# Kernel tuning notes

Measured on AMD Instinct MI355X. Metric: run time of the kernel, lower is better.

The kernel has to match this reference:

```python
import jax, jax.numpy as jnp
import numpy as np

V, E, H, M = 50000, 256, 512, 100   # vocab, emb_dim, hid_dim, mlp_hid_dim
H2 = H // 2                          # per-direction GRU size
B, S, T = 64, 400, 25                # batch, src_len, max_trg_len
EOS = 2                              # vocab['</s>'] -> CE weight 0


def _gru(x, h, Wih, Whh, bih, bhh):
    # torch GRU/GRUCell gate math
    gi = x @ Wih.T + bih
    gh = h @ Whh.T + bhh
    ir, iz, inn = jnp.split(gi, 3, axis=-1)
    hr, hz, hn = jnp.split(gh, 3, axis=-1)
    r = jax.nn.sigmoid(ir + hr)
    z = jax.nn.sigmoid(iz + hz)
    n = jnp.tanh(inn + r * hn)
    return (1.0 - z) * n + z * h


def _run_gru(xs, Wih, Whh, bih, bhh, reverse):
    # xs: [S, B, E] -> ys [S, B, H2], hT [B, H2]
    if reverse:
        xs = xs[::-1]
    h0 = jnp.zeros((xs.shape[1], Whh.shape[1]), xs.dtype)
    def step(h, x):
        h2 = _gru(x, h, Wih, Whh, bih, bhh)
        return h2, h2
    hT, ys = jax.lax.scan(step, h0, xs)
    if reverse:
        ys = ys[::-1]
    return ys, hT


def _model(src, trg, params):
    (emb, Wih_f, Whh_f, bih_f, bhh_f, Wih_b, Whh_b, bih_b, bhh_b,
     W1, b1, W2, b2, Wd, bd, We, be, Wo, bo,
     Wih_c, Whh_c, bih_c, bhh_c, Wv, bv) = params
    # ---- encode ----
    embeds = emb[src].transpose(1, 0, 2)                    # [S, B, E]
    ys_f, hf = _run_gru(embeds, Wih_f, Whh_f, bih_f, bhh_f, False)
    ys_b, hb = _run_gru(embeds, Wih_b, Whh_b, bih_b, bhh_b, True)
    states = jnp.concatenate([ys_f, ys_b], axis=-1)         # [S, B, H]
    enc_hidden = jnp.concatenate([hf, hb], axis=-1)         # [B, H]
    sgate = jax.nn.sigmoid(states @ W1.T + b1 + (enc_hidden @ W2.T + b2)[None])
    states = states * sgate
    enc_proj = states @ We.T + be                           # [S, B, M] (loop-invariant)
    # ---- decode (training path, weighted CE per step) ----
    def dec_step(carry, tok):
        h, loss = carry
        wemb = emb[tok]                                     # [B, E]
        e = jnp.tanh((h @ Wd.T + bd)[None] + enc_proj) @ Wo.T + bo  # [S, B, 1]
        a = jax.nn.softmax(e, axis=0)
        c = jnp.sum(a * states, axis=0)                     # [B, H]
        h2 = _gru(jnp.concatenate([c, wemb], axis=-1), h, Wih_c, Whh_c, bih_c, bhh_c)
        logits = h2 @ Wv.T + bv                             # [B, V]
        logp = jax.nn.log_softmax(logits, axis=-1)
        nll = -jnp.take_along_axis(logp, tok[:, None], axis=1)[:, 0]
        w = (tok != EOS).astype(logits.dtype)               # CE class weight mask
        step_loss = jnp.sum(w * nll) / jnp.sum(w)           # torch weighted-mean CE
        return (h2, loss + step_loss), None
    toks = trg[:, : T - 1].T                                # [T-1, B]
    (_, loss), _ = jax.lax.scan(dec_step, (enc_hidden, jnp.zeros((), states.dtype)), toks)
    return loss / B


def setup_inputs() -> dict:
    key = jax.random.key(0)
    ks = jax.random.split(key, 16)
    def p(k, shape, s=0.05):
        return jax.random.normal(k, shape, jnp.float32) * s
    z = lambda n: jnp.zeros((n,), jnp.float32)
    return {
        "src": jax.random.randint(ks[0], (B, S), 0, V, dtype=jnp.int32),
        "trg": jax.random.randint(ks[1], (B, T), 0, V, dtype=jnp.int32),
        "emb": p(ks[2], (V, E)),
        "Wih_f": p(ks[3], (3 * H2, E)), "Whh_f": p(ks[4], (3 * H2, H2)),
        "bih_f": z(3 * H2), "bhh_f": z(3 * H2),
        "Wih_b": p(ks[5], (3 * H2, E)), "Whh_b": p(ks[6], (3 * H2, H2)),
        "bih_b": z(3 * H2), "bhh_b": z(3 * H2),
        "W1": p(ks[7], (H, H)), "b1": z(H),
        "W2": p(ks[8], (H, H)), "b2": z(H),
        "Wd": p(ks[9], (M, H)), "bd": z(M),
        "We": p(ks[10], (M, H)), "be": z(M),
        "Wo": p(ks[11], (1, M)), "bo": z(1),
        "Wih_c": p(ks[12], (3 * H, H + E)), "Whh_c": p(ks[13], (3 * H, H)),
        "bih_c": z(3 * H), "bhh_c": z(3 * H),
        "Wv": p(ks[14], (V, H)), "bv": z(V),
    }


def reference(src, trg, emb, Wih_f, Whh_f, bih_f, bhh_f, Wih_b, Whh_b, bih_b, bhh_b,
              W1, b1, W2, b2, Wd, bd, We, be, Wo, bo,
              Wih_c, Whh_c, bih_c, bhh_c, Wv, bv):
    params = (emb, Wih_f, Whh_f, bih_f, bhh_f, Wih_b, Whh_b, bih_b, bhh_b,
              W1, b1, W2, b2, Wd, bd, We, be, Wo, bo,
              Wih_c, Whh_c, bih_c, bhh_c, Wv, bv)
    return _model(src, trg, params)
```

## Files before the change

### kernel.cpp

```cpp
#include <hip/hip_runtime.h>

typedef __bf16 bf16;
typedef bf16 bf16x2 __attribute__((ext_vector_type(2)));
typedef bf16 bf16x4 __attribute__((ext_vector_type(4)));
typedef bf16 bf16x8 __attribute__((ext_vector_type(8)));
typedef float f32x4 __attribute__((ext_vector_type(4)));

#define DEVFN __device__ __forceinline__

constexpr int cV = 50000, cE = 256, cH = 512, cM = 100, cH2 = 256;
constexpr int cB = 64, cS = 400, cT = 25, cEOS = 2;
constexpr int cSB = cS * cB;
constexpr int cG2 = 3 * cH2;
constexpr int cGP = 772;
constexpr int cKcat = 1280;
constexpr int cN4 = 2048;
constexpr int cNTV = (cV + 63) / 64;
constexpr int cTD = cT - 1;
constexpr int cVT = cV / 16;

constexpr size_t OFF_WV = 0;
constexpr size_t N_WV = (size_t)cV * cH;
constexpr size_t OFF_WIHF = OFF_WV + N_WV;
constexpr size_t N_WIH = (size_t)cG2 * cE;
constexpr size_t OFF_WHHF = OFF_WIHF + N_WIH;
constexpr size_t N_WHH = (size_t)cG2 * cH2;
constexpr size_t OFF_WIHB = OFF_WHHF + N_WHH;
constexpr size_t OFF_WHHB = OFF_WIHB + N_WIH;
constexpr size_t OFF_W1 = OFF_WHHB + N_WHH;
constexpr size_t N_WSQ = (size_t)cH * cH;
constexpr size_t OFF_W2 = OFF_W1 + N_WSQ;
constexpr size_t OFF_WE = OFF_W2 + N_WSQ;
constexpr size_t N_WE = (size_t)cM * cH;
constexpr size_t TOT_W = OFF_WE + N_WE;

constexpr int NB_CVT = (int)(TOT_W / 4 / 256);
constexpr int NB_WP = cN4 * cKcat / 256;
constexpr int NB_GATHER = cSB * cE / 256;
constexpr int NB_PREP = NB_CVT + NB_WP + NB_GATHER;

struct GArgs {
  const bf16* A; const bf16* Bw; const float* bias;
  float* outF; bf16* outBf;
  const float* auxF; const bf16* auxBf;
  int M, N, K, ldo;
};

DEVFN float sigm(float x) { return 1.f / (1.f + __expf(-x)); }
DEVFN float tanh_f(float x) {
  float e2 = __expf(2.f * x);
  return 1.f - 2.f / (e2 + 1.f);
}

DEVFN void gload_lds16(const void* g, void* l) {
  __builtin_amdgcn_global_load_lds(
      (const __attribute__((address_space(1))) void*)g,
      (__attribute__((address_space(3))) void*)l, 16, 0, 0);
}

template <int EPI>
__global__ __launch_bounds__(256) void gemm64_k(GArgs g) {
  const int tid = threadIdx.x;
  const int w = blockIdx.x * 4 + (tid >> 6);
  const int tM = g.M >> 6;
  const int tN = (g.N + 63) >> 6;
  if (w >= tM * tN) return;
  const int im = w % tM, in = w / tM;
  const int m0 = im << 6, n0 = in << 6;
  const int lane = tid & 63, lr = lane & 15, lh = lane >> 4;

  f32x4 acc[4][4];
#pragma unroll
  for (int i = 0; i < 4; ++i)
#pragma unroll
    for (int j = 0; j < 4; ++j)
#pragma unroll
      for (int r = 0; r < 4; ++r) acc[i][j][r] = 0.f;

  bf16x8 bz;
#pragma unroll
  for (int q = 0; q < 8; ++q) bz[q] = (bf16)0.f;

  const int K = g.K;
#pragma unroll 2
  for (int k0 = 0; k0 < K; k0 += 32) {
    bf16x8 av[4], bw[4];
#pragma unroll
    for (int mt = 0; mt < 4; ++mt)
      av[mt] = *(const bf16x8*)(g.A + (size_t)(m0 + mt * 16 + lr) * K + k0 + lh * 8);
#pragma unroll
    for (int nt = 0; nt < 4; ++nt) {
      int row = n0 + nt * 16 + lr;
      bw[nt] = (row < g.N) ? *(const bf16x8*)(g.Bw + (size_t)row * K + k0 + lh * 8) : bz;
    }
#pragma unroll
    for (int mt = 0; mt < 4; ++mt)
#pragma unroll
      for (int nt = 0; nt < 4; ++nt)
        acc[mt][nt] = __builtin_amdgcn_mfma_f32_16x16x32_bf16(av[mt], bw[nt], acc[mt][nt], 0, 0, 0);
  }

#pragma unroll
  for (int mt = 0; mt < 4; ++mt) {
#pragma unroll
    for (int nt = 0; nt < 4; ++nt) {
      const int n = n0 + nt * 16 + lr;
      if (n < g.N) {
        const float bia = g.bias[n];
#pragma unroll
        for (int r = 0; r < 4; ++r) {
          const int m = m0 + mt * 16 + lh * 4 + r;
          float v = acc[mt][nt][r] + bia;
          if constexpr (EPI == 0) {
            g.outF[(size_t)m * g.ldo + n] = v;
          } else {
            float sg = sigm(v + g.auxF[(size_t)(m & 63) * g.ldo + n]);
            float st = (float)g.auxBf[(size_t)m * g.ldo + n];
            g.outBf[(size_t)m * g.ldo + n] = (bf16)(sg * st);
          }
        }
      }
    }
  }
}

__global__ void prep_k(const float* __restrict__ wv, const float* __restrict__ wihf,
                       const float* __restrict__ whhf, const float* __restrict__ wihb,
                       const float* __restrict__ whhb, const float* __restrict__ w1,
                       const float* __restrict__ w2, const float* __restrict__ we,
                       bf16* __restrict__ dst,
                       const float* __restrict__ Wih_c, const float* __restrict__ Whh_c,
                       const float* __restrict__ bih_c, const float* __restrict__ bhh_c,
                       bf16* __restrict__ Wp, float* __restrict__ bp,
                       const int* __restrict__ src, const float* __restrict__ emb,
                       bf16* __restrict__ embeds) {
  const int blk = blockIdx.x, tid = threadIdx.x;

  if (blk < NB_CVT) {
    size_t i = ((size_t)blk * 256 + tid) * 4;
    if (i >= TOT_W) return;
    if (i < OFF_WIHF) {
      float4 v = *(const float4*)(wv + i);
      size_t row = i >> 9, col = i & 511;
      size_t tile = row >> 4, lr = row & 15, kc = col >> 5, lh = (col >> 3) & 3, e = col & 7;
      size_t d = ((tile * 16 + kc) * 64 + lr * 4 + lh) * 8 + e;
      bf16x4 o;
      o[0] = (bf16)v.x; o[1] = (bf16)v.y; o[2] = (bf16)v.z; o[3] = (bf16)v.w;
      *(bf16x4*)(dst + d) = o;
      return;
    }
    const float* s;
    size_t off;
    if (i < OFF_WHHF) { s = wihf; off = OFF_WIHF; }
    else if (i < OFF_WIHB) { s = whhf; off = OFF_WHHF; }
    else if (i < OFF_WHHB) { s = wihb; off = OFF_WIHB; }
    else if (i < OFF_W1) { s = whhb; off = OFF_WHHB; }
    else if (i < OFF_W2) { s = w1; off = OFF_W1; }
    else if (i < OFF_WE) { s = w2; off = OFF_W2; }
    else { s = we; off = OFF_WE; }
    float4 v = *(const float4*)(s + (i - off));
    bf16x4 o;
    o[0] = (bf16)v.x; o[1] = (bf16)v.y; o[2] = (bf16)v.z; o[3] = (bf16)v.w;
    *(bf16x4*)(dst + i) = o;
    return;
  }
  if (blk < NB_CVT + NB_WP) {
    int i = (blk - NB_CVT) * 256 + tid;
    int j = i / cKcat, c = i % cKcat;
    int bi = j >> 6, gg = (j >> 4) & 3, idx = j & 15;
    int u = bi * 16 + idx;
    float v;
    if (gg == 0) v = (c < 768) ? Wih_c[(size_t)u * 768 + c] : Whh_c[(size_t)u * 512 + (c - 768)];
    else if (gg == 1) v = (c < 768) ? Wih_c[(size_t)(512 + u) * 768 + c] : Whh_c[(size_t)(512 + u) * 512 + (c - 768)];
    else if (gg == 2) v = (c < 768) ? Wih_c[(size_t)(1024 + u) * 768 + c] : 0.f;
    else v = (c < 768) ? 0.f : Whh_c[(size_t)(1024 + u) * 512 + (c - 768)];
    {
      size_t tile = (size_t)j >> 4, lr = j & 15, kc = c >> 5, lh = (c >> 3) & 3, e = c & 7;
      Wp[((tile * 40 + kc) * 64 + lr * 4 + lh) * 8 + e] = (bf16)v;
    }
    if (c == 0) {
      float bb;
      if (gg == 0) bb = bih_c[u] + bhh_c[u];
      else if (gg == 1) bb = bih_c[512 + u] + bhh_c[512 + u];
      else if (gg == 2) bb = bih_c[1024 + u];
      else bb = bhh_c[1024 + u];
      bp[j] = bb;
    }
    return;
  }
  {
    int i = (blk - NB_CVT - NB_WP) * 256 + tid;
    int e = i & 255;
    int sb = i >> 8;
    int s = sb >> 6, b = sb & 63;
    int tok = src[b * cS + s];
    embeds[i] = (bf16)emb[(size_t)tok * cE + e];
  }
}

__global__ __launch_bounds__(256) void gi2_k(const bf16* __restrict__ embeds,
                                             const bf16* __restrict__ WihF,
                                             const float* __restrict__ bihF,
                                             float* __restrict__ giF,
                                             const bf16* __restrict__ WihB,
                                             const float* __restrict__ bihB,
                                             float* __restrict__ giB) {
  int blk = blockIdx.x;
  const bf16* Bw;
  const float* bias;
  float* outF;
  if (blk < 1200) { Bw = WihF; bias = bihF; outF = giF; }
  else { blk -= 1200; Bw = WihB; bias = bihB; outF = giB; }
  const int tid = threadIdx.x;
  const int w = blk * 4 + (tid >> 6);
  const int im = w % 400, in = w / 400;
  const int m0 = im << 6, n0 = in << 6;
  const int lane = tid & 63, lr = lane & 15, lh = lane >> 4;

  f32x4 acc[4][4];
#pragma unroll
  for (int i = 0; i < 4; ++i)
#pragma unroll
    for (int j = 0; j < 4; ++j)
#pragma unroll
      for (int r = 0; r < 4; ++r) acc[i][j][r] = 0.f;

#pragma unroll 2
  for (int k0 = 0; k0 < cE; k0 += 32) {
    bf16x8 av[4], bw[4];
#pragma unroll
    for (int mt = 0; mt < 4; ++mt)
      av[mt] = *(const bf16x8*)(embeds + (size_t)(m0 + mt * 16 + lr) * cE + k0 + lh * 8);
#pragma unroll
    for (int nt = 0; nt < 4; ++nt)
      bw[nt] = *(const bf16x8*)(Bw + (size_t)(n0 + nt * 16 + lr) * cE + k0 + lh * 8);
#pragma unroll
    for (int mt = 0; mt < 4; ++mt)
#pragma unroll
      for (int nt = 0; nt < 4; ++nt)
        acc[mt][nt] = __builtin_amdgcn_mfma_f32_16x16x32_bf16(av[mt], bw[nt], acc[mt][nt], 0, 0, 0);
  }
#pragma unroll
  for (int mt = 0; mt < 4; ++mt)
#pragma unroll
    for (int nt = 0; nt < 4; ++nt) {
      const int n = n0 + nt * 16 + lr;
      const float bia = bias[n];
#pragma unroll
      for (int r = 0; r < 4; ++r) {
        const int m = m0 + mt * 16 + lh * 4 + r;
        outF[(size_t)m * cG2 + n] = acc[mt][nt][r] + bia;
      }
    }
}

__global__ __launch_bounds__(512, 1) void enc_rnn_k(
    const bf16* __restrict__ WhhF, const bf16* __restrict__ WhhB,
    const float* __restrict__ giF, const float* __restrict__ giB,
    const float* __restrict__ bhhF, const float* __restrict__ bhhB,
    bf16* __restrict__ hdec0_bf, float* __restrict__ hdec0_f,
    bf16* __restrict__ states) {
  const int blk = blockIdx.x;
  const int dir = blk >> 2;
  const int bc = blk & 3;
  const bf16* Whh = dir ? WhhB : WhhF;
  const float* gi = dir ? giB : giF;
  const float* bhh = dir ? bhhB : bhhF;

  const int tid = threadIdx.x;
  const int lane = tid & 63, w = tid >> 6;
  const int lr = lane & 15, lh = lane >> 4;
  const int u0 = w * 32;

  bf16x8 Bf[6][8];
  float bh[6];
#pragma unroll
  for (int gg = 0; gg < 3; ++gg)
#pragma unroll
    for (int ut = 0; ut < 2; ++ut) {
      int nbase = gg * 256 + u0 + ut * 16;
#pragma unroll
      for (int kf = 0; kf < 8; ++kf)
        Bf[gg * 2 + ut][kf] = *(const bf16x8*)(Whh + (size_t)(nbase + lr) * 256 + kf * 32 + lh * 8);
      bh[gg * 2 + ut] = bhh[nbase + lr];
    }

  __shared__ float gilds[2][16][cGP];
  __shared__ bf16 hs[2][16][264];

  auto prefetch = [&](int t2) {
    if (t2 >= cS) return;
    const int s2 = dir ? (cS - 1 - t2) : t2;
    const int buf = t2 & 1;
#pragma unroll
    for (int rr2 = 0; rr2 < 2; ++rr2) {
      const int row = w * 2 + rr2;
      const char* srcb = (const char*)(gi + ((size_t)s2 * cB + bc * 16 + row) * cG2);
      char* dstb = (char*)&gilds[buf][row][0];
#pragma unroll
      for (int c = 0; c < 3; ++c)
        gload_lds16(srcb + c * 1024 + lane * 16, dstb + c * 1024);
    }
  };

  float hreg[2][4];
#pragma unroll
  for (int ut = 0; ut < 2; ++ut)
#pragma unroll
    for (int r = 0; r < 4; ++r) hreg[ut][r] = 0.f;

  prefetch(0);
  for (int i = tid; i < 16 * 264; i += 512) ((bf16*)hs[0])[i] = (bf16)0.f;
  __syncthreads();

  for (int t = 0; t < cS; ++t) {
    const int buf = t & 1, nbuf = buf ^ 1;
    prefetch(t + 1);

    bf16x8 av[8];
#pragma unroll
    for (int kf = 0; kf < 8; ++kf)
      av[kf] = *(const bf16x8*)(&hs[buf][lr][kf * 32 + lh * 8]);

    float gir[2][4], giz[2][4], gin[2][4];
#pragma unroll
    for (int ut = 0; ut < 2; ++ut) {
      const int u = u0 + ut * 16 + lr;
#pragma unroll
      for (int r = 0; r < 4; ++r) {
        const int b = lh * 4 + r;
        gir[ut][r] = gilds[buf][b][u];
        giz[ut][r] = gilds[buf][b][256 + u];
        gin[ut][r] = gilds[buf][b][512 + u];
      }
    }

    f32x4 acc[6];
#pragma unroll
    for (int j = 0; j < 6; ++j)
#pragma unroll
      for (int r = 0; r < 4; ++r) acc[j][r] = 0.f;

#pragma unroll
    for (int kf = 0; kf < 8; ++kf)
#pragma unroll
      for (int nt = 0; nt < 6; ++nt)
        acc[nt] = __builtin_amdgcn_mfma_f32_16x16x32_bf16(av[kf], Bf[nt][kf], acc[nt], 0, 0, 0);

#pragma unroll
    for (int ut = 0; ut < 2; ++ut) {
      const int u = u0 + ut * 16 + lr;
#pragma unroll
      for (int r = 0; r < 4; ++r) {
        const int b = lh * 4 + r;
        float rr = sigm(gir[ut][r] + acc[ut][r] + bh[ut]);
        float zz = sigm(giz[ut][r] + acc[2 + ut][r] + bh[2 + ut]);
        float nn = tanh_f(gin[ut][r] + rr * (acc[4 + ut][r] + bh[4 + ut]));
        float hnew = (1.f - zz) * nn + zz * hreg[ut][r];
        hreg[ut][r] = hnew;
        hs[nbuf][b][u] = (bf16)hnew;
      }
    }

    __syncthreads();

    {
      const int s_src = dir ? (cS - 1 - t) : t;
      const int row = tid >> 5, c8 = tid & 31;
      bf16x8 v = *(const bf16x8*)(&hs[nbuf][row][c8 * 8]);
      *(bf16x8*)(states + ((size_t)s_src * cB + bc * 16 + row) * cH + dir * 256 + c8 * 8) = v;
    }
  }

#pragma unroll
  for (int ut = 0; ut < 2; ++ut)
#pragma unroll
    for (int r = 0; r < 4; ++r) {
      const int b = bc * 16 + lh * 4 + r;
      const int col = dir * 256 + u0 + ut * 16 + lr;
      hdec0_f[(size_t)b * cH + col] = hreg[ut][r];
      hdec0_bf[(size_t)b * cH + col] = (bf16)hreg[ut][r];
    }
}

__global__ __launch_bounds__(256) void projtransp_k(const bf16* __restrict__ statesg,
                                                    const bf16* __restrict__ We_b,
                                                    const float* __restrict__ be,
                                                    float* __restrict__ epT,
                                                    bf16* __restrict__ sgT) {
  __shared__ bf16 tile[64][520];
  const int tid = threadIdx.x;
  if (blockIdx.x < 200) {
    const int w = blockIdx.x * 4 + (tid >> 6);
    const int im = w % 400, in = w / 400;
    const int m0 = im << 6, n0 = in << 6;
    const int lane = tid & 63, lr = lane & 15, lh = lane >> 4;
    f32x4 acc[4][4];
#pragma unroll
    for (int i = 0; i < 4; ++i)
#pragma unroll
      for (int j = 0; j < 4; ++j)
#pragma unroll
        for (int r = 0; r < 4; ++r) acc[i][j][r] = 0.f;
    bf16x8 bz;
#pragma unroll
    for (int q = 0; q < 8; ++q) bz[q] = (bf16)0.f;
#pragma unroll 2
    for (int k0 = 0; k0 < cH; k0 += 32) {
      bf16x8 av[4], bw[4];
#pragma unroll
      for (int mt = 0; mt < 4; ++mt)
        av[mt] = *(const bf16x8*)(statesg + (size_t)(m0 + mt * 16 + lr) * cH + k0 + lh * 8);
#pragma unroll
      for (int nt = 0; nt < 4; ++nt) {
        int row = n0 + nt * 16 + lr;
        bw[nt] = (row < cM) ? *(const bf16x8*)(We_b + (size_t)row * cH + k0 + lh * 8) : bz;
      }
#pragma unroll
      for (int mt = 0; mt < 4; ++mt)
#pragma unroll
        for (int nt = 0; nt < 4; ++nt)
          acc[mt][nt] = __builtin_amdgcn_mfma_f32_16x16x32_bf16(av[mt], bw[nt], acc[mt][nt], 0, 0, 0);
    }
#pragma unroll
    for (int mt = 0; mt < 4; ++mt)
#pragma unroll
      for (int nt = 0; nt < 4; ++nt) {
        const int n = n0 + nt * 16 + lr;
        if (n < cM) {
          const float bia = be[n];
#pragma unroll
          for (int r = 0; r < 4; ++r) {
            const int m = m0 + mt * 16 + lh * 4 + r;
            const int bb = m & 63, s = m >> 6;
            epT[((size_t)bb * cM + n) * cS + s] = acc[mt][nt][r] + bia;
          }
        }
      }
    return;
  }
  const int b = blockIdx.x - 200;
  for (int s0 = 0; s0 < cS; s0 += 64) {
    __syncthreads();
    for (int c = tid; c < 64 * 64; c += 256) {
      int row = c >> 6, col = c & 63;
      *(bf16x8*)(&tile[row][col * 8]) =
          *(const bf16x8*)(statesg + ((size_t)(s0 + row) * cB + b) * cH + col * 8);
    }
    __syncthreads();
    for (int c = tid; c < 512 * 8; c += 256) {
      int k = c >> 3, sc = c & 7;
      bf16x8 v;
#pragma unroll
      for (int j = 0; j < 8; ++j) v[j] = tile[sc * 8 + j][k];
      *(bf16x8*)(sgT + ((size_t)b * cH + k) * cS + s0 + sc * 8) = v;
    }
  }
}

__global__ __launch_bounds__(512) void attn_k(
    const bf16* __restrict__ hin, const float* __restrict__ Wd, const float* __restrict__ bd,
    const float* __restrict__ Wo, const float* __restrict__ bo,
    const float* __restrict__ epT, const bf16* __restrict__ sgT,
    const float* __restrict__ emb, const int* __restrict__ trg, int t,
    bf16* __restrict__ xh) {
  const int b = blockIdx.x, tid = threadIdx.x;
  const int lane = tid & 63, wid = tid >> 6;
  __shared__ float hsh[512];
  __shared__ float dsh[100];
  __shared__ float esh[400];
  __shared__ float red[32];
  __shared__ float wos[100];

  if (tid < 100) wos[tid] = Wo[tid];
  hsh[tid] = (float)hin[b * 512 + tid];
  __syncthreads();

  for (int j = wid; j < 100; j += 8) {
    const float* wr = Wd + (size_t)j * 512 + lane * 8;
    float a = 0.f;
#pragma unroll
    for (int q = 0; q < 8; ++q) a += wr[q] * hsh[lane * 8 + q];
#pragma unroll
    for (int m = 1; m < 64; m <<= 1) a += __shfl_xor(a, m);
    if (lane == 0) dsh[j] = a + bd[j];
  }
  __syncthreads();

  float e0 = -3.4e38f;
  if (tid < 400) {
    const float* p = epT + (size_t)b * cM * cS + tid;
    float a0 = 0.f, a1 = 0.f, a2 = 0.f, a3 = 0.f;
#pragma unroll
    for (int j = 0; j < 100; j += 4) {
      a0 += wos[j + 0] * tanh_f(dsh[j + 0] + p[(j + 0) * cS]);
      a1 += wos[j + 1] * tanh_f(dsh[j + 1] + p[(j + 1) * cS]);
      a2 += wos[j + 2] * tanh_f(dsh[j + 2] + p[(j + 2) * cS]);
      a3 += wos[j + 3] * tanh_f(dsh[j + 3] + p[(j + 3) * cS]);
    }
    e0 = bo[0] + ((a0 + a1) + (a2 + a3));
  }
  float mx = e0;
#pragma unroll
  for (int m = 1; m < 64; m <<= 1) mx = fmaxf(mx, __shfl_xor(mx, m));
  if (lane == 0) red[wid] = mx;
  __syncthreads();
  mx = red[0];
#pragma unroll
  for (int q = 1; q < 8; ++q) mx = fmaxf(mx, red[q]);

  float av = (tid < 400) ? __expf(e0 - mx) : 0.f;
  if (tid < 400) esh[tid] = av;
  float sm = av;
#pragma unroll
  for (int m = 1; m < 64; m <<= 1) sm += __shfl_xor(sm, m);
  if (lane == 0) red[8 + wid] = sm;
  __syncthreads();
  sm = red[8];
#pragma unroll
  for (int q = 1; q < 8; ++q) sm += red[8 + q];
  const float inv = 1.f / sm;

  {
    const bf16* sp = sgT + ((size_t)b * cH + tid) * cS;
    float c0 = 0.f, c1 = 0.f, c2 = 0.f, c3 = 0.f;
    for (int s = 0; s < 384; s += 32) {
      bf16x8 v0 = *(const bf16x8*)(sp + s);
      bf16x8 v1 = *(const bf16x8*)(sp + s + 8);
      bf16x8 v2 = *(const bf16x8*)(sp + s + 16);
      bf16x8 v3 = *(const bf16x8*)(sp + s + 24);
#pragma unroll
      for (int j = 0; j < 8; ++j) {
        c0 += esh[s + j] * (float)v0[j];
        c1 += esh[s + 8 + j] * (float)v1[j];
        c2 += esh[s + 16 + j] * (float)v2[j];
        c3 += esh[s + 24 + j] * (float)v3[j];
      }
    }
    {
      bf16x8 v0 = *(const bf16x8*)(sp + 384);
      bf16x8 v1 = *(const bf16x8*)(sp + 392);
#pragma unroll
      for (int j = 0; j < 8; ++j) {
        c0 += esh[384 + j] * (float)v0[j];
        c1 += esh[392 + j] * (float)v1[j];
      }
    }
    xh[(size_t)b * cKcat + tid] = (bf16)(((c0 + c1) + (c2 + c3)) * inv);
  }
  if (tid < 256) {
    const int tok = trg[b * cT + t];
    xh[(size_t)b * cKcat + 512 + tid] = (bf16)emb[(size_t)tok * cE + tid];
  }
  xh[(size_t)b * cKcat + 768 + tid] = hin[b * 512 + tid];
}

__global__ __launch_bounds__(256) void gru_k(
    const bf16* __restrict__ xh, const bf16* __restrict__ Wp, const float* __restrict__ bp,
    const float* __restrict__ hin_f, float* __restrict__ hout_f, bf16* __restrict__ hallt) {
  const int tid = threadIdx.x;
  const int lane = tid & 63, wid = tid >> 6;
  const int w = blockIdx.x * 4 + wid;
  const int n0 = w << 6, lr = lane & 15, lh = lane >> 4;
  f32x4 acc[4][4];
#pragma unroll
  for (int i = 0; i < 4; ++i)
#pragma unroll
    for (int j = 0; j < 4; ++j)
#pragma unroll
      for (int r = 0; r < 4; ++r) acc[i][j][r] = 0.f;
#pragma unroll 2
  for (int k0 = 0; k0 < cKcat; k0 += 32) {
    bf16x8 av[4], bw[4];
#pragma unroll
    for (int mt = 0; mt < 4; ++mt)
      av[mt] = *(const bf16x8*)(xh + (size_t)(mt * 16 + lr) * cKcat + k0 + lh * 8);
#pragma unroll
    for (int nt = 0; nt < 4; ++nt)
      bw[nt] = *(const bf16x8*)(Wp + (((size_t)(w * 4 + nt) * 40 + (k0 >> 5)) * 64 + lr * 4 + lh) * 8);
#pragma unroll
    for (int mt = 0; mt < 4; ++mt)
#pragma unroll
      for (int nt = 0; nt < 4; ++nt)
        acc[mt][nt] = __builtin_amdgcn_mfma_f32_16x16x32_bf16(av[mt], bw[nt], acc[mt][nt], 0, 0, 0);
  }
  const int u = (n0 >> 2) + lr;
  const float br = bp[n0 + lr];
  const float bz2 = bp[n0 + 16 + lr];
  const float bi2 = bp[n0 + 32 + lr];
  const float bh2 = bp[n0 + 48 + lr];
#pragma unroll
  for (int mt = 0; mt < 4; ++mt)
#pragma unroll
    for (int r = 0; r < 4; ++r) {
      const int bb = mt * 16 + lh * 4 + r;
      float rr = sigm(acc[mt][0][r] + br);
      float zz = sigm(acc[mt][1][r] + bz2);
      float nn = tanh_f(acc[mt][2][r] + bi2 + rr * (acc[mt][3][r] + bh2));
      float h2v = (1.f - zz) * nn + zz * hin_f[(size_t)bb * cH + u];
      hout_f[(size_t)bb * cH + u] = h2v;
      hallt[(size_t)bb * cH + u] = (bf16)h2v;
    }
}

__global__ __launch_bounds__(256) void biglogits_k(
    const bf16* __restrict__ hall, const bf16* __restrict__ WvS,
    const float* __restrict__ bv, float* __restrict__ partials) {
  const int tid = threadIdx.x;
  const int lane = tid & 63, wid = tid >> 6;
  const int im = blockIdx.x % cTD;
  const int in = (blockIdx.x / cTD) * 4 + wid;
  if (in >= cNTV) return;
  const int m0 = im << 6, lr = lane & 15, lh = lane >> 4;

  f32x4 acc[4][4];
#pragma unroll
  for (int i = 0; i < 4; ++i)
#pragma unroll
    for (int j = 0; j < 4; ++j)
#pragma unroll
      for (int r = 0; r < 4; ++r) acc[i][j][r] = 0.f;
  bf16x8 bz;
#pragma unroll
  for (int q = 0; q < 8; ++q) bz[q] = (bf16)0.f;

#pragma unroll 2
  for (int k0 = 0; k0 < cH; k0 += 32) {
    bf16x8 av[4], bw[4];
#pragma unroll
    for (int mt = 0; mt < 4; ++mt)
      av[mt] = *(const bf16x8*)(hall + (size_t)(m0 + mt * 16 + lr) * cH + k0 + lh * 8);
#pragma unroll
    for (int nt = 0; nt < 4; ++nt) {
      const int tile = in * 4 + nt;
      bw[nt] = (tile < cVT)
                   ? *(const bf16x8*)(WvS + (((size_t)tile * 16 + (k0 >> 5)) * 64 + lr * 4 + lh) * 8)
                   : bz;
    }
#pragma unroll
    for (int mt = 0; mt < 4; ++mt)
#pragma unroll
      for (int nt = 0; nt < 4; ++nt)
        acc[mt][nt] = __builtin_amdgcn_mfma_f32_16x16x32_bf16(av[mt], bw[nt], acc[mt][nt], 0, 0, 0);
  }

#pragma unroll
  for (int mt = 0; mt < 4; ++mt) {
#pragma unroll
    for (int r = 0; r < 4; ++r) {
      const int m = m0 + mt * 16 + lh * 4 + r;
      float vv[4];
      float mx = -3.4e38f;
#pragma unroll
      for (int nt = 0; nt < 4; ++nt) {
        int n = (in << 6) + nt * 16 + lr;
        float v = (n < cV) ? (acc[mt][nt][r] + bv[n]) : -3.4e38f;
        vv[nt] = v;
        mx = fmaxf(mx, v);
      }
#pragma unroll
      for (int msk = 1; msk < 16; msk <<= 1) mx = fmaxf(mx, __shfl_xor(mx, msk));
      float sm = 0.f;
#pragma unroll
      for (int nt = 0; nt < 4; ++nt) {
        int n = (in << 6) + nt * 16 + lr;
        if (n < cV) sm += __expf(vv[nt] - mx);
      }
#pragma unroll
      for (int msk = 1; msk < 16; msk <<= 1) sm += __shfl_xor(sm, msk);
      if (lr == 0) {
        float* p = partials + ((size_t)m * cNTV + in) * 2;
        p[0] = mx;
        p[1] = sm;
      }
    }
  }
}

__global__ __launch_bounds__(64) void rowloss_all_k(
    const float* __restrict__ partials, const bf16* __restrict__ hall,
    const float* __restrict__ Wv, const float* __restrict__ bv,
    const int* __restrict__ trg, float* __restrict__ rnll, float* __restrict__ rw) {
  const int m = blockIdx.x, tid = threadIdx.x;
  const int t = m >> 6, bb = m & 63;
  float mx = -3.4e38f, sm = 0.f;
  const float* pr = partials + (size_t)m * cNTV * 2;
  for (int p = tid; p < cNTV; p += 64) {
    float m2 = pr[p * 2], s2 = pr[p * 2 + 1];
    if (m2 > mx) { sm = sm * __expf(mx - m2) + s2; mx = m2; }
    else sm += s2 * __expf(m2 - mx);
  }
#pragma unroll
  for (int msk = 1; msk < 64; msk <<= 1) {
    float om = __shfl_xor(mx, msk), os = __shfl_xor(sm, msk);
    if (om > mx) { sm = sm * __expf(mx - om) + os; mx = om; }
    else sm += os * __expf(om - mx);
  }
  const int tok = trg[bb * cT + t];
  float dot = 0.f;
  {
    const float* wr = Wv + (size_t)tok * cH + tid * 8;
    const bf16* hr = hall + (size_t)m * cH + tid * 8;
    bf16x8 h8 = *(const bf16x8*)hr;
#pragma unroll
    for (int j = 0; j < 8; ++j) dot += (float)h8[j] * wr[j];
  }
#pragma unroll
  for (int msk = 1; msk < 64; msk <<= 1) dot += __shfl_xor(dot, msk);
  if (tid == 0) {
    float lse = mx + __logf(sm);
    float nll = lse - (dot + bv[tok]);
    float wgt = (tok != cEOS) ? 1.f : 0.f;
    rnll[m] = wgt * nll;
    rw[m] = wgt;
  }
}

__global__ __launch_bounds__(64) void final_loss_k(const float* __restrict__ rnll,
                                                   const float* __restrict__ rw,
                                                   float* __restrict__ out) {
  __shared__ float sl[32];
  const int t = threadIdx.x;
  if (t < cTD) {
    float a = 0.f, d = 0.f;
    for (int b = 0; b < cB; ++b) { a += rnll[t * cB + b]; d += rw[t * cB + b]; }
    sl[t] = a / d;
  }
  __syncthreads();
  if (t == 0) {
    float s = 0.f;
    for (int i = 0; i < cTD; ++i) s += sl[i];
    out[0] = s / (float)cB;
  }
}

extern "C" void kernel_launch(void* const* d_in, const int* in_sizes, int n_in,
                              void* d_out, int out_size, void* d_ws, size_t ws_size,
                              hipStream_t stream) {
  (void)in_sizes; (void)n_in; (void)out_size; (void)ws_size;
  const int* src = (const int*)d_in[0];
  const int* trg = (const int*)d_in[1];
  const float* emb = (const float*)d_in[2];
  const float* Wih_f = (const float*)d_in[3];
  const float* Whh_f = (const float*)d_in[4];
  const float* bih_f = (const float*)d_in[5];
  const float* bhh_f = (const float*)d_in[6];
  const float* Wih_b = (const float*)d_in[7];
  const float* Whh_b = (const float*)d_in[8];
  const float* bih_b = (const float*)d_in[9];
  const float* bhh_b = (const float*)d_in[10];
  const float* W1 = (const float*)d_in[11];
  const float* b1 = (const float*)d_in[12];
  const float* W2 = (const float*)d_in[13];
  const float* b2 = (const float*)d_in[14];
  const float* Wd = (const float*)d_in[15];
  const float* bd = (const float*)d_in[16];
  const float* We = (const float*)d_in[17];
  const float* be = (const float*)d_in[18];
  const float* Wo = (const float*)d_in[19];
  const float* bo = (const float*)d_in[20];
  const float* Wih_c = (const float*)d_in[21];
  const float* Whh_c = (const float*)d_in[22];
  const float* bih_c = (const float*)d_in[23];
  const float* bhh_c = (const float*)d_in[24];
  const float* Wv = (const float*)d_in[25];
  const float* bv = (const float*)d_in[26];
  float* out = (float*)d_out;

  char* ws = (char*)d_ws;
  size_t off = 0;
  auto carve = [&](size_t bytes) -> void* {
    void* p = ws + off;
    off += (bytes + 255) & ~(size_t)255;
    return p;
  };
  bf16* wcat = (bf16*)carve(TOT_W * 2);
  bf16* WvS = wcat + OFF_WV;
  bf16* Wihf_b = wcat + OFF_WIHF;
  bf16* Whhf_b = wcat + OFF_WHHF;
  bf16* Wihb_b = wcat + OFF_WIHB;
  bf16* Whhb_b = wcat + OFF_WHHB;
  bf16* W1_b = wcat + OFF_W1;
  bf16* W2_b = wcat + OFF_W2;
  bf16* We_b = wcat + OFF_WE;
  bf16* Wp_b = (bf16*)carve((size_t)cN4 * cKcat * 2);
  float* bp = (float*)carve((size_t)cN4 * 4);
  bf16* embeds = (bf16*)carve((size_t)cSB * cE * 2);
  float* gi_f = (float*)carve((size_t)cSB * cG2 * 4);
  float* gi_b = (float*)carve((size_t)cSB * cG2 * 4);
  bf16* states = (bf16*)carve((size_t)cSB * cH * 2);
  bf16* statesg = (bf16*)carve((size_t)cSB * cH * 2);
  bf16* statesgT = (bf16*)carve((size_t)cSB * cH * 2);
  bf16* hdec0_bf = (bf16*)carve((size_t)cB * cH * 2);
  float* hdec0_f = (float*)carve((size_t)cB * cH * 4);
  float* hfA = (float*)carve((size_t)cB * cH * 4);
  float* hfB = (float*)carve((size_t)cB * cH * 4);
  float* hw2 = (float*)carve((size_t)cB * cH * 4);
  float* epT = (float*)carve((size_t)cB * cM * cS * 4);
  bf16* xh = (bf16*)carve((size_t)cB * cKcat * 2);
  bf16* hall = (bf16*)carve((size_t)cTD * cB * cH * 2);
  float* partials = (float*)carve((size_t)cTD * cB * cNTV * 2 * 4);
  float* rnll = (float*)carve((size_t)cTD * cB * 4);
  float* rw = (float*)carve((size_t)cTD * cB * 4);

  prep_k<<<dim3(NB_PREP), dim3(256), 0, stream>>>(
      Wv, Wih_f, Whh_f, Wih_b, Whh_b, W1, W2, We, wcat,
      Wih_c, Whh_c, bih_c, bhh_c, Wp_b, bp, src, emb, embeds);
  gi2_k<<<dim3(2400), dim3(256), 0, stream>>>(embeds, Wihf_b, bih_f, gi_f,
                                              Wihb_b, bih_b, gi_b);
  enc_rnn_k<<<dim3(8), dim3(512), 0, stream>>>(Whhf_b, Whhb_b, gi_f, gi_b, bhh_f, bhh_b,
                                               hdec0_bf, hdec0_f, states);
  {
    GArgs ga{hdec0_bf, W2_b, b2, hw2, nullptr, nullptr, nullptr, cB, cH, cH, cH};
    gemm64_k<0><<<dim3(2), dim3(256), 0, stream>>>(ga);
  }
  {
    GArgs ga{states, W1_b, b1, nullptr, statesg, hw2, states, cSB, cH, cH, cH};
    int waves = (cSB / 64) * (cH / 64);
    gemm64_k<1><<<dim3((waves + 3) / 4), dim3(256), 0, stream>>>(ga);
  }
  projtransp_k<<<dim3(264), dim3(256), 0, stream>>>(statesg, We_b, be, epT, statesgT);

  for (int t = 0; t < cTD; ++t) {
    const bf16* hin_bf = (t == 0) ? hdec0_bf : (hall + (size_t)(t - 1) * cB * cH);
    const float* hin_f = (t == 0) ? hdec0_f : ((t & 1) ? hfA : hfB);
    float* hout_f = (t & 1) ? hfB : hfA;

    attn_k<<<dim3(cB), dim3(512), 0, stream>>>(hin_bf, Wd, bd, Wo, bo, epT, statesgT,
                                               emb, trg, t, xh);
    gru_k<<<dim3(8), dim3(256), 0, stream>>>(xh, Wp_b, bp, hin_f, hout_f,
                                             hall + (size_t)t * cB * cH);
  }

  biglogits_k<<<dim3(cTD * ((cNTV + 3) / 4)), dim3(256), 0, stream>>>(hall, WvS, bv, partials);
  rowloss_all_k<<<dim3(cTD * cB), dim3(64), 0, stream>>>(partials, hall, Wv, bv, trg, rnll, rw);
  final_loss_k<<<dim3(1), dim3(64), 0, stream>>>(rnll, rw, out);
}
```

Measured before the change: 3.677 ms.

## Overlap weight conversion with encoder RNN and store attention projection in bf16

```diff
diff --git a/kernel.cpp b/kernel.cpp
--- a/kernel.cpp
+++ b/kernel.cpp
@@ -34,10 +34,16 @@
 constexpr size_t N_WE = (size_t)cM * cH;
 constexpr size_t TOT_W = OFF_WE + N_WE;
 
-constexpr int NB_CVT = (int)(TOT_W / 4 / 256);
-constexpr int NB_WP = cN4 * cKcat / 256;
+constexpr int NB_CVT1 = (int)(4 * N_WIH / 4 / 256);
 constexpr int NB_GATHER = cSB * cE / 256;
-constexpr int NB_PREP = NB_CVT + NB_WP + NB_GATHER;
+constexpr int NB_PREP1 = NB_CVT1 + NB_GATHER;
+
+constexpr int NB_WVS = (int)(N_WV / 4 / 512);
+constexpr size_t N_TAIL = N_WSQ + N_WSQ + N_WE;
+constexpr int NB_TAIL = (int)(N_TAIL / 4 / 512);
+constexpr int NB_WP2 = cN4 * cKcat / 4 / 512;
+constexpr int NB_PREP2 = NB_WVS + NB_TAIL + NB_WP2;
+constexpr int ENC_GRID = 8 + NB_PREP2;
 
 struct GArgs {
   const bf16* A; const bf16* Bw; const float* bias;
@@ -124,72 +130,28 @@
   }
 }
 
-__global__ void prep_k(const float* __restrict__ wv, const float* __restrict__ wihf,
-                       const float* __restrict__ whhf, const float* __restrict__ wihb,
-                       const float* __restrict__ whhb, const float* __restrict__ w1,
-                       const float* __restrict__ w2, const float* __restrict__ we,
-                       bf16* __restrict__ dst,
-                       const float* __restrict__ Wih_c, const float* __restrict__ Whh_c,
-                       const float* __restrict__ bih_c, const float* __restrict__ bhh_c,
-                       bf16* __restrict__ Wp, float* __restrict__ bp,
-                       const int* __restrict__ src, const float* __restrict__ emb,
-                       bf16* __restrict__ embeds) {
+__global__ void prep1_k(const float* __restrict__ wihf, const float* __restrict__ whhf,
+                        const float* __restrict__ wihb, const float* __restrict__ whhb,
+                        bf16* __restrict__ dst,
+                        const int* __restrict__ src, const float* __restrict__ emb,
+                        bf16* __restrict__ embeds) {
   const int blk = blockIdx.x, tid = threadIdx.x;
-
-  if (blk < NB_CVT) {
-    size_t i = ((size_t)blk * 256 + tid) * 4;
-    if (i >= TOT_W) return;
-    if (i < OFF_WIHF) {
-      float4 v = *(const float4*)(wv + i);
-      size_t row = i >> 9, col = i & 511;
-      size_t tile = row >> 4, lr = row & 15, kc = col >> 5, lh = (col >> 3) & 3, e = col & 7;
-      size_t d = ((tile * 16 + kc) * 64 + lr * 4 + lh) * 8 + e;
-      bf16x4 o;
-      o[0] = (bf16)v.x; o[1] = (bf16)v.y; o[2] = (bf16)v.z; o[3] = (bf16)v.w;
-      *(bf16x4*)(dst + d) = o;
-      return;
-    }
+  if (blk < NB_CVT1) {
+    size_t i = ((size_t)blk * 256 + tid) * 4 + OFF_WIHF;
     const float* s;
     size_t off;
     if (i < OFF_WHHF) { s = wihf; off = OFF_WIHF; }
     else if (i < OFF_WIHB) { s = whhf; off = OFF_WHHF; }
     else if (i < OFF_WHHB) { s = wihb; off = OFF_WIHB; }
-    else if (i < OFF_W1) { s = whhb; off = OFF_WHHB; }
-    else if (i < OFF_W2) { s = w1; off = OFF_W1; }
-    else if (i < OFF_WE) { s = w2; off = OFF_W2; }
-    else { s = we; off = OFF_WE; }
+    else { s = whhb; off = OFF_WHHB; }
     float4 v = *(const float4*)(s + (i - off));
     bf16x4 o;
     o[0] = (bf16)v.x; o[1] = (bf16)v.y; o[2] = (bf16)v.z; o[3] = (bf16)v.w;
     *(bf16x4*)(dst + i) = o;
     return;
   }
-  if (blk < NB_CVT + NB_WP) {
-    int i = (blk - NB_CVT) * 256 + tid;
-    int j = i / cKcat, c = i % cKcat;
-    int bi = j >> 6, gg = (j >> 4) & 3, idx = j & 15;
-    int u = bi * 16 + idx;
-    float v;
-    if (gg == 0) v = (c < 768) ? Wih_c[(size_t)u * 768 + c] : Whh_c[(size_t)u * 512 + (c - 768)];
-    else if (gg == 1) v = (c < 768) ? Wih_c[(size_t)(512 + u) * 768 + c] : Whh_c[(size_t)(512 + u) * 512 + (c - 768)];
-    else if (gg == 2) v = (c < 768) ? Wih_c[(size_t)(1024 + u) * 768 + c] : 0.f;
-    else v = (c < 768) ? 0.f : Whh_c[(size_t)(1024 + u) * 512 + (c - 768)];
-    {
-      size_t tile = (size_t)j >> 4, lr = j & 15, kc = c >> 5, lh = (c >> 3) & 3, e = c & 7;
-      Wp[((tile * 40 + kc) * 64 + lr * 4 + lh) * 8 + e] = (bf16)v;
-    }
-    if (c == 0) {
-      float bb;
-      if (gg == 0) bb = bih_c[u] + bhh_c[u];
-      else if (gg == 1) bb = bih_c[512 + u] + bhh_c[512 + u];
-      else if (gg == 2) bb = bih_c[1024 + u];
-      else bb = bhh_c[1024 + u];
-      bp[j] = bb;
-    }
-    return;
-  }
   {
-    int i = (blk - NB_CVT - NB_WP) * 256 + tid;
+    int i = (blk - NB_CVT1) * 256 + tid;
     int e = i & 255;
     int sb = i >> 8;
     int s = sb >> 6, b = sb & 63;
@@ -259,7 +221,71 @@
     const float* __restrict__ giF, const float* __restrict__ giB,
     const float* __restrict__ bhhF, const float* __restrict__ bhhB,
     bf16* __restrict__ hdec0_bf, float* __restrict__ hdec0_f,
-    bf16* __restrict__ states) {
+    bf16* __restrict__ states,
+    const float* __restrict__ wv, const float* __restrict__ w1,
+    const float* __restrict__ w2, const float* __restrict__ we,
+    bf16* __restrict__ wcat,
+    const float* __restrict__ Wih_c, const float* __restrict__ Whh_c,
+    const float* __restrict__ bih_c, const float* __restrict__ bhh_c,
+    bf16* __restrict__ Wp, float* __restrict__ bp) {
+  const int tid = threadIdx.x;
+
+  if (blockIdx.x >= 8) {
+    const int pb = blockIdx.x - 8;
+    if (pb < NB_WVS) {
+      size_t i = ((size_t)pb * 512 + tid) * 4;
+      float4 v = *(const float4*)(wv + i);
+      size_t row = i >> 9, col = i & 511;
+      size_t tile = row >> 4, lr = row & 15, kc = col >> 5, lh = (col >> 3) & 3, e = col & 7;
+      size_t d = ((tile * 16 + kc) * 64 + lr * 4 + lh) * 8 + e;
+      bf16x4 o;
+      o[0] = (bf16)v.x; o[1] = (bf16)v.y; o[2] = (bf16)v.z; o[3] = (bf16)v.w;
+      *(bf16x4*)(wcat + d) = o;
+      return;
+    }
+    if (pb < NB_WVS + NB_TAIL) {
+      size_t i = ((size_t)(pb - NB_WVS) * 512 + tid) * 4 + OFF_W1;
+      const float* s;
+      size_t off;
+      if (i < OFF_W2) { s = w1; off = OFF_W1; }
+      else if (i < OFF_WE) { s = w2; off = OFF_W2; }
+      else { s = we; off = OFF_WE; }
+      float4 v = *(const float4*)(s + (i - off));
+      bf16x4 o;
+      o[0] = (bf16)v.x; o[1] = (bf16)v.y; o[2] = (bf16)v.z; o[3] = (bf16)v.w;
+      *(bf16x4*)(wcat + i) = o;
+      return;
+    }
+    {
+      size_t i0 = ((size_t)(pb - NB_WVS - NB_TAIL) * 512 + tid) * 4;
+#pragma unroll
+      for (int q = 0; q < 4; ++q) {
+        size_t i = i0 + q;
+        int j = (int)(i / cKcat), c = (int)(i % cKcat);
+        int bi = j >> 6, gg = (j >> 4) & 3, idx = j & 15;
+        int u = bi * 16 + idx;
+        float v;
+        if (gg == 0) v = (c < 768) ? Wih_c[(size_t)u * 768 + c] : Whh_c[(size_t)u * 512 + (c - 768)];
+        else if (gg == 1) v = (c < 768) ? Wih_c[(size_t)(512 + u) * 768 + c] : Whh_c[(size_t)(512 + u) * 512 + (c - 768)];
+        else if (gg == 2) v = (c < 768) ? Wih_c[(size_t)(1024 + u) * 768 + c] : 0.f;
+        else v = (c < 768) ? 0.f : Whh_c[(size_t)(1024 + u) * 512 + (c - 768)];
+        {
+          size_t tile = (size_t)j >> 4, lr = j & 15, kc = c >> 5, lh = (c >> 3) & 3, e = c & 7;
+          Wp[((tile * 40 + kc) * 64 + lr * 4 + lh) * 8 + e] = (bf16)v;
+        }
+        if (c == 0) {
+          float bb;
+          if (gg == 0) bb = bih_c[u] + bhh_c[u];
+          else if (gg == 1) bb = bih_c[512 + u] + bhh_c[512 + u];
+          else if (gg == 2) bb = bih_c[1024 + u];
+          else bb = bhh_c[1024 + u];
+          bp[j] = bb;
+        }
+      }
+      return;
+    }
+  }
+
   const int blk = blockIdx.x;
   const int dir = blk >> 2;
   const int bc = blk & 3;
@@ -267,7 +293,6 @@
   const float* gi = dir ? giB : giF;
   const float* bhh = dir ? bhhB : bhhF;
 
-  const int tid = threadIdx.x;
   const int lane = tid & 63, w = tid >> 6;
   const int lr = lane & 15, lh = lane >> 4;
   const int u0 = w * 32;
@@ -386,7 +411,7 @@
 __global__ __launch_bounds__(256) void projtransp_k(const bf16* __restrict__ statesg,
                                                     const bf16* __restrict__ We_b,
                                                     const float* __restrict__ be,
-                                                    float* __restrict__ epT,
+                                                    bf16* __restrict__ epT,
                                                     bf16* __restrict__ sgT) {
   __shared__ bf16 tile[64][520];
   const int tid = threadIdx.x;
@@ -433,7 +458,7 @@
           for (int r = 0; r < 4; ++r) {
             const int m = m0 + mt * 16 + lh * 4 + r;
             const int bb = m & 63, s = m >> 6;
-            epT[((size_t)bb * cM + n) * cS + s] = acc[mt][nt][r] + bia;
+            epT[((size_t)bb * cM + n) * cS + s] = (bf16)(acc[mt][nt][r] + bia);
           }
         }
       }
@@ -461,17 +486,25 @@
 __global__ __launch_bounds__(512) void attn_k(
     const bf16* __restrict__ hin, const float* __restrict__ Wd, const float* __restrict__ bd,
     const float* __restrict__ Wo, const float* __restrict__ bo,
-    const float* __restrict__ epT, const bf16* __restrict__ sgT,
+    const bf16* __restrict__ epT, const bf16* __restrict__ sgT,
     const float* __restrict__ emb, const int* __restrict__ trg, int t,
     bf16* __restrict__ xh) {
   const int b = blockIdx.x, tid = threadIdx.x;
   const int lane = tid & 63, wid = tid >> 6;
+  __shared__ bf16 epl[100][408];
   __shared__ float hsh[512];
   __shared__ float dsh[100];
   __shared__ float esh[400];
   __shared__ float red[32];
   __shared__ float wos[100];
 
+  {
+    const bf16* src = epT + (size_t)b * cM * cS;
+    for (int c = tid; c < 100 * 50; c += 512) {
+      int j = c / 50, ch = c % 50;
+      *(bf16x8*)(&epl[j][ch * 8]) = *(const bf16x8*)(src + (size_t)j * cS + ch * 8);
+    }
+  }
   if (tid < 100) wos[tid] = Wo[tid];
   hsh[tid] = (float)hin[b * 512 + tid];
   __syncthreads();
@@ -489,14 +522,13 @@
 
   float e0 = -3.4e38f;
   if (tid < 400) {
-    const float* p = epT + (size_t)b * cM * cS + tid;
     float a0 = 0.f, a1 = 0.f, a2 = 0.f, a3 = 0.f;
 #pragma unroll
     for (int j = 0; j < 100; j += 4) {
-      a0 += wos[j + 0] * tanh_f(dsh[j + 0] + p[(j + 0) * cS]);
-      a1 += wos[j + 1] * tanh_f(dsh[j + 1] + p[(j + 1) * cS]);
-      a2 += wos[j + 2] * tanh_f(dsh[j + 2] + p[(j + 2) * cS]);
-      a3 += wos[j + 3] * tanh_f(dsh[j + 3] + p[(j + 3) * cS]);
+      a0 += wos[j + 0] * tanh_f(dsh[j + 0] + (float)epl[j + 0][tid]);
+      a1 += wos[j + 1] * tanh_f(dsh[j + 1] + (float)epl[j + 1][tid]);
+      a2 += wos[j + 2] * tanh_f(dsh[j + 2] + (float)epl[j + 2][tid]);
+      a3 += wos[j + 3] * tanh_f(dsh[j + 3] + (float)epl[j + 3][tid]);
     }
     e0 = bo[0] + ((a0 + a1) + (a2 + a3));
   }
@@ -523,18 +555,26 @@
 
   {
     const bf16* sp = sgT + ((size_t)b * cH + tid) * cS;
-    float c0 = 0.f, c1 = 0.f, c2 = 0.f, c3 = 0.f;
-    for (int s = 0; s < 384; s += 32) {
+    float c0 = 0.f, c1 = 0.f, c2 = 0.f, c3 = 0.f, c4 = 0.f, c5 = 0.f, c6 = 0.f, c7 = 0.f;
+    for (int s = 0; s < 384; s += 64) {
       bf16x8 v0 = *(const bf16x8*)(sp + s);
       bf16x8 v1 = *(const bf16x8*)(sp + s + 8);
       bf16x8 v2 = *(const bf16x8*)(sp + s + 16);
       bf16x8 v3 = *(const bf16x8*)(sp + s + 24);
+      bf16x8 v4 = *(const bf16x8*)(sp + s + 32);
+      bf16x8 v5 = *(const bf16x8*)(sp + s + 40);
+      bf16x8 v6 = *(const bf16x8*)(sp + s + 48);
+      bf16x8 v7 = *(const bf16x8*)(sp + s + 56);
 #pragma unroll
       for (int j = 0; j < 8; ++j) {
         c0 += esh[s + j] * (float)v0[j];
         c1 += esh[s + 8 + j] * (float)v1[j];
         c2 += esh[s + 16 + j] * (float)v2[j];
         c3 += esh[s + 24 + j] * (float)v3[j];
+        c4 += esh[s + 32 + j] * (float)v4[j];
+        c5 += esh[s + 40 + j] * (float)v5[j];
+        c6 += esh[s + 48 + j] * (float)v6[j];
+        c7 += esh[s + 56 + j] * (float)v7[j];
       }
     }
     {
@@ -546,7 +586,8 @@
         c1 += esh[392 + j] * (float)v1[j];
       }
     }
-    xh[(size_t)b * cKcat + tid] = (bf16)(((c0 + c1) + (c2 + c3)) * inv);
+    float cc = (((c0 + c1) + (c2 + c3)) + ((c4 + c5) + (c6 + c7)));
+    xh[(size_t)b * cKcat + tid] = (bf16)(cc * inv);
   }
   if (tid < 256) {
     const int tok = trg[b * cT + t];
@@ -796,20 +837,20 @@
   float* hfA = (float*)carve((size_t)cB * cH * 4);
   float* hfB = (float*)carve((size_t)cB * cH * 4);
   float* hw2 = (float*)carve((size_t)cB * cH * 4);
-  float* epT = (float*)carve((size_t)cB * cM * cS * 4);
+  bf16* epT = (bf16*)carve((size_t)cB * cM * cS * 2);
   bf16* xh = (bf16*)carve((size_t)cB * cKcat * 2);
   bf16* hall = (bf16*)carve((size_t)cTD * cB * cH * 2);
   float* partials = (float*)carve((size_t)cTD * cB * cNTV * 2 * 4);
   float* rnll = (float*)carve((size_t)cTD * cB * 4);
   float* rw = (float*)carve((size_t)cTD * cB * 4);
 
-  prep_k<<<dim3(NB_PREP), dim3(256), 0, stream>>>(
-      Wv, Wih_f, Whh_f, Wih_b, Whh_b, W1, W2, We, wcat,
-      Wih_c, Whh_c, bih_c, bhh_c, Wp_b, bp, src, emb, embeds);
+  prep1_k<<<dim3(NB_PREP1), dim3(256), 0, stream>>>(
+      Wih_f, Whh_f, Wih_b, Whh_b, wcat, src, emb, embeds);
   gi2_k<<<dim3(2400), dim3(256), 0, stream>>>(embeds, Wihf_b, bih_f, gi_f,
                                               Wihb_b, bih_b, gi_b);
-  enc_rnn_k<<<dim3(8), dim3(512), 0, stream>>>(Whhf_b, Whhb_b, gi_f, gi_b, bhh_f, bhh_b,
-                                               hdec0_bf, hdec0_f, states);
+  enc_rnn_k<<<dim3(ENC_GRID), dim3(512), 0, stream>>>(
+      Whhf_b, Whhb_b, gi_f, gi_b, bhh_f, bhh_b, hdec0_bf, hdec0_f, states,
+      Wv, W1, W2, We, wcat, Wih_c, Whh_c, bih_c, bhh_c, Wp_b, bp);
   {
     GArgs ga{hdec0_bf, W2_b, b2, hw2, nullptr, nullptr, nullptr, cB, cH, cH, cH};
     gemm64_k<0><<<dim3(2), dim3(256), 0, stream>>>(ga);
```

Result: slower. 3.914 ms (+6.5%).
